# Kernel optimization log

Measured on AMD Instinct MI355X. Metric: run time of the kernel, lower is better.

Reference implementation:

```python
import jax, jax.numpy as jnp
import numpy as np

EPS = 1e-12  # layer_norm_eps

def _ln(h, g, b):
    m = jnp.mean(h, axis=-1, keepdims=True)
    v = jnp.var(h, axis=-1, keepdims=True)
    return (h - m) / jnp.sqrt(v + EPS) * g + b

def setup_inputs() -> dict:
    key = jax.random.key(0)
    B, L, C, N = 32, 512, 256, 16
    ks = jax.random.split(key, 8)
    f = jax.random.normal
    return {
        'query': f(ks[0], (B, L, C), jnp.float32),
        'x': f(ks[1], (B, L, C), jnp.float32),
        'offset': f(ks[2], (B, L, 2 * N), jnp.float32) * 0.1,
        'w1': f(ks[3], (L, L // 4), jnp.float32) * 0.02, 'b1': jnp.zeros((L // 4,), jnp.float32),
        'g1': jnp.ones((L // 4,), jnp.float32), 'bt1': jnp.zeros((L // 4,), jnp.float32),
        'w2': f(ks[4], (L // 4, L), jnp.float32) * 0.02, 'b2': jnp.zeros((L,), jnp.float32),
        'w3': f(ks[5], (C, C), jnp.float32) * 0.02, 'b3': jnp.zeros((C,), jnp.float32),
        'g3': jnp.ones((C,), jnp.float32), 'bt3': jnp.zeros((C,), jnp.float32),
        'w4': f(ks[6], (C, 2 * N), jnp.float32) * 0.02, 'b4': jnp.zeros((2 * N,), jnp.float32),
    }

def reference(query, x, offset, w1, b1, g1, bt1, w2, b2, w3, b3, g3, bt3, w4, b4):
    B, L, C = x.shape
    N = w4.shape[1] // 2
    # sample_layer: Linear over the sequence axis (query permuted to [B,C,L])
    q = jnp.swapaxes(query, 1, 2)                                        # [B,C,L]
    q = jax.nn.gelu(_ln(q @ w1 + b1, g1, bt1), approximate=False) @ w2 + b2
    q = jnp.swapaxes(q, 1, 2)                                            # [B,L,C]
    # adjust_layer over channels -> per-step 2N offsets, tanh * 0.02
    adj = jax.nn.gelu(_ln(q @ w3 + b3, g3, bt3), approximate=False) @ w4 + b4
    adj = jnp.tanh(adj) * 0.02                                           # [B,L,2N]
    local = (offset + adj).reshape(B, L, N, 2)
    # precomputed reference points (x-coord 0, y-coord depends on query step i)
    i = jnp.arange(L, dtype=x.dtype)
    n = jnp.arange(N, dtype=x.dtype) + 0.5
    ref_y = n[None, :] * 2.0 * (i[:, None] + 1e-9) / (N * L) - 1.0       # [L,N]
    ref = jnp.stack([jnp.zeros_like(ref_y), ref_y], axis=-1)             # [L,N,2]
    pos = jnp.tanh(local + ref[None])                                    # [B,L,N,2]
    # grid_sample equivalent: input [B*L, C, H=L, W=1], align_corners=True,
    # bilinear, zero padding. With W=1 the x-coordinate always maps to col 0,
    # so only pos[...,1] matters. Causal mask zeroes keys h > query step l
    # before sampling; since bilinear sampling is linear in the input, we mask
    # the two gathered taps instead of materializing the O(B*L*L*C) tensor.
    pix = (pos[..., 1] + 1.0) * 0.5 * (L - 1)                            # [B,L,N]
    i0f = jnp.floor(pix)
    frac = pix - i0f
    i0 = i0f.astype(jnp.int32)
    i1 = i0 + 1
    lpos = jnp.arange(L, dtype=jnp.int32)[None, :, None]
    v0 = (i0 >= 0) & (i0 < L) & (i0 <= lpos)
    v1 = (i1 >= 0) & (i1 < L) & (i1 <= lpos)
    c0 = jnp.clip(i0, 0, L - 1)
    c1 = jnp.clip(i1, 0, L - 1)
    bidx = jnp.arange(B)[:, None, None]
    val0 = x[bidx, c0]                                                   # [B,L,N,C]
    val1 = x[bidx, c1]                                                   # [B,L,N,C]
    w0 = jnp.where(v0, 1.0 - frac, 0.0)
    w1_ = jnp.where(v1, frac, 0.0)
    out = w0[..., None] * val0 + w1_[..., None] * val1                   # [B,L,N,C]
    return (out, offset, pos)
```

## Files before the change

### kernel.cpp

```cpp
#include <hip/hip_runtime.h>
#include <hip/hip_fp16.h>
#include <math.h>


typedef _Float16 f16;
typedef _Float16 f16x8 __attribute__((ext_vector_type(8)));
typedef float f32x4 __attribute__((ext_vector_type(4)));

#define ZERO4 f32x4{0.f, 0.f, 0.f, 0.f}

__device__ __forceinline__ float gelu_exact(float v) {
  return 0.5f * v * (1.0f + erff(v * 0.70710678118654752f));
}

__global__ __launch_bounds__(256) void k0_prep(
    const float* __restrict__ w1, const float* __restrict__ w2,
    const float* __restrict__ w3, const float* __restrict__ w4,
    f16* __restrict__ w1T, f16* __restrict__ w2T,
    f16* __restrict__ w3T, f16* __restrict__ w4T) {
  __shared__ f16 tile[64][80];
  int blk = blockIdx.x;
  const int tid = threadIdx.x;
  const float* in; f16* out; int R, Cc, tr, tc;
  if (blk < 16)      { in = w1; out = w1T; R = 512; Cc = 128; tr = blk >> 1; tc = blk & 1; }
  else if (blk < 32) { blk -= 16; in = w2; out = w2T; R = 128; Cc = 512; tr = blk >> 3; tc = blk & 7; }
  else if (blk < 48) { blk -= 32; in = w3; out = w3T; R = 256; Cc = 256; tr = blk >> 2; tc = blk & 3; }
  else               { blk -= 48; in = w4; out = w4T; R = 256; Cc = 32;  tr = blk;      tc = 0; }
  const int r0 = tr * 64, c0 = tc * 64;
  for (int id = tid; id < 4096; id += 256) {
    int rr = id >> 6, cc = id & 63;
    if (c0 + cc < Cc) tile[cc][rr] = (f16)in[(r0 + rr) * Cc + c0 + cc];
  }
  __syncthreads();
  for (int id = tid; id < 512; id += 256) {
    int cc = id >> 3, ch = id & 7;
    if (c0 + cc < Cc)
      *(f16x8*)(out + (c0 + cc) * R + r0 + ch * 8) = *(f16x8*)&tile[cc][ch * 8];
  }
}

__global__ __launch_bounds__(256) void k12_sample(
    const float* __restrict__ query, const f16* __restrict__ w1T,
    const f16* __restrict__ w2T,
    const float* __restrict__ b1, const float* __restrict__ g1,
    const float* __restrict__ bt1, const float* __restrict__ b2,
    f16* __restrict__ qout) {
  __shared__ char pool[38912];
  const int tid = threadIdx.x;
  const int b = blockIdx.x >> 4;
  const int c0 = (blockIdx.x & 15) << 4;
  const int lane = tid & 63, w = tid >> 6;
  const int mrow = lane & 15, kg = lane >> 4;
  char* At = pool;
  char* Bt = pool + 2048;
  char* t1s = pool + 32768;
  float* sb2 = (float*)(pool + 36864);

  sb2[tid] = b2[tid];
  sb2[tid + 256] = b2[tid + 256];

  const int qll = tid >> 4, qcc = tid & 15;
  const int wrj = tid >> 3, wch = tid & 7;

  float qv[4]; f16x8 wv[4];
#pragma unroll
  for (int it = 0; it < 4; ++it) {
    qv[it] = query[(((b << 9) + 0 + qll + it * 16) << 8) + c0 + qcc];
    wv[it] = *(const f16x8*)(w1T + (wrj + it * 32) * 512 + 0 + wch * 8);
  }

  f32x4 acc[2] = {ZERO4, ZERO4};
  for (int s = 0; s < 8; ++s) {
#pragma unroll
    for (int it = 0; it < 4; ++it) {
      int ll = qll + it * 16;
      *(f16*)(At + qcc * 128 + ((2 * ll) ^ ((qcc & 7) << 4))) = (f16)qv[it];
    }
#pragma unroll
    for (int it = 0; it < 4; ++it) {
      int rj = wrj + it * 32;
      *(f16x8*)(Bt + rj * 128 + ((wch * 16) ^ ((rj & 7) << 4))) = wv[it];
    }
    __syncthreads();
    if (s < 7) {
      const int k0n = (s + 1) << 6;
#pragma unroll
      for (int it = 0; it < 4; ++it) {
        qv[it] = query[(((b << 9) + k0n + qll + it * 16) << 8) + c0 + qcc];
        wv[it] = *(const f16x8*)(w1T + (wrj + it * 32) * 512 + k0n + wch * 8);
      }
    }
#pragma unroll
    for (int kk = 0; kk < 2; ++kk) {
      f16x8 a = *(const f16x8*)(At + mrow * 128 + (((kk << 6) + (kg << 4)) ^ ((mrow & 7) << 4)));
#pragma unroll
      for (int nf = 0; nf < 2; ++nf) {
        int rn = w * 32 + nf * 16 + mrow;
        f16x8 bfr = *(const f16x8*)(Bt + rn * 128 + (((kk << 6) + (kg << 4)) ^ ((rn & 7) << 4)));
        acc[nf] = __builtin_amdgcn_mfma_f32_16x16x32_f16(a, bfr, acc[nf], 0, 0, 0);
      }
    }
    __syncthreads();
  }

  f16x8 av[8];
#pragma unroll
  for (int it = 0; it < 8; ++it)
    av[it] = *(const f16x8*)(w2T + ((tid >> 4) + it * 16) * 128 + (tid & 15) * 8);

  float (*hs)[132] = (float(*)[132])pool;
#pragma unroll
  for (int nf = 0; nf < 2; ++nf)
#pragma unroll
    for (int i = 0; i < 4; ++i)
      hs[kg * 4 + i][w * 32 + nf * 16 + mrow] = acc[nf][i];
  __syncthreads();
  {
    const int r = tid >> 4, g = tid & 15;
    float s1 = 0.f, s2 = 0.f, vals[8];
#pragma unroll
    for (int jj = 0; jj < 8; ++jj) {
      int j = g * 8 + jj;
      float v = hs[r][j] + b1[j];
      vals[jj] = v; s1 += v; s2 += v * v;
    }
#pragma unroll
    for (int m = 1; m < 16; m <<= 1) { s1 += __shfl_xor(s1, m, 64); s2 += __shfl_xor(s2, m, 64); }
    const float mean = s1 * (1.f / 128.f);
    float var = fmaxf(s2 * (1.f / 128.f) - mean * mean, 0.f);
    const float rstd = rsqrtf(var + 1e-12f);
    f16 ov[8];
#pragma unroll
    for (int jj = 0; jj < 8; ++jj) {
      int j = g * 8 + jj;
      float v = (vals[jj] - mean) * rstd * g1[j] + bt1[j];
      ov[jj] = (f16)gelu_exact(v);
    }
    __syncthreads();
    *(f16x8*)(t1s + r * 256 + ((g * 16) ^ ((r & 7) << 4))) = *(f16x8*)ov;
  }
  __syncthreads();

  char* At2 = pool;
  const int ar2 = tid >> 4, ac2 = tid & 15;
  for (int lc = 0; lc < 4; ++lc) {
#pragma unroll
    for (int it = 0; it < 8; ++it) {
      int r = ar2 + it * 16;
      *(f16x8*)(At2 + r * 256 + ((ac2 * 16) ^ ((r & 7) << 4))) = av[it];
    }
    __syncthreads();
    if (lc < 3) {
#pragma unroll
      for (int it = 0; it < 8; ++it)
        av[it] = *(const f16x8*)(w2T + ((lc + 1) * 128 + ar2 + it * 16) * 128 + ac2 * 8);
    }
    f32x4 acc2[2] = {ZERO4, ZERO4};
#pragma unroll
    for (int ks = 0; ks < 4; ++ks) {
      f16x8 bfr = *(const f16x8*)(t1s + mrow * 256 + (((ks << 6) + (kg << 4)) ^ ((mrow & 7) << 4)));
#pragma unroll
      for (int mf = 0; mf < 2; ++mf) {
        int rm = w * 32 + mf * 16 + mrow;
        f16x8 a = *(const f16x8*)(At2 + rm * 256 + (((ks << 6) + (kg << 4)) ^ ((rm & 7) << 4)));
        acc2[mf] = __builtin_amdgcn_mfma_f32_16x16x32_f16(a, bfr, acc2[mf], 0, 0, 0);
      }
    }
#pragma unroll
    for (int mf = 0; mf < 2; ++mf)
#pragma unroll
      for (int i = 0; i < 4; ++i) {
        int l = lc * 128 + w * 32 + mf * 16 + kg * 4 + i;
        qout[((b << 9) + l) * 256 + c0 + mrow] = (f16)(acc2[mf][i] + sb2[l]);
      }
    __syncthreads();
  }
}

__global__ __launch_bounds__(256) void k3_adjust(
    const f16* __restrict__ qbuf, const f16* __restrict__ w3T,
    const float* __restrict__ b3, const float* __restrict__ g3,
    const float* __restrict__ bt3, const f16* __restrict__ w4T,
    const float* __restrict__ b4, const float* __restrict__ offset,
    float* __restrict__ off_out, float* __restrict__ pos_out) {
  __shared__ char pool[34816];
  __shared__ char w4t[32 * 512];
  __shared__ float sb3[256];
  const int tid = threadIdx.x;
  const int b = blockIdx.x >> 5;
  const int l0 = (blockIdx.x & 31) << 4;
  const int lane = tid & 63, w = tid >> 6;
  const int mrow = lane & 15, kg = lane >> 4;
  char* At = pool;
  char* Bt = pool + 2048;

  for (int id = tid; id < 1024; id += 256) {
    int r = id >> 5, c = id & 31;
    f16x8 v = *(const f16x8*)(w4T + r * 256 + c * 8);
    *(f16x8*)(w4t + r * 512 + ((c * 16) ^ ((r & 7) << 4))) = v;
  }
  sb3[tid] = b3[tid];

  const int sr = tid >> 3, sc = tid & 7;
  f16x8 aq; f16x8 bq[8];
  if (tid < 128) aq = *(const f16x8*)(qbuf + ((b << 9) + l0 + sr) * 256 + 0 + sc * 8);
#pragma unroll
  for (int it = 0; it < 8; ++it)
    bq[it] = *(const f16x8*)(w3T + (sr + it * 32) * 256 + 0 + sc * 8);

  f32x4 acc[4] = {ZERO4, ZERO4, ZERO4, ZERO4};
  for (int s = 0; s < 4; ++s) {
    if (tid < 128)
      *(f16x8*)(At + sr * 128 + ((sc * 16) ^ ((sr & 7) << 4))) = aq;
#pragma unroll
    for (int it = 0; it < 8; ++it) {
      int r = sr + it * 32;
      *(f16x8*)(Bt + r * 128 + ((sc * 16) ^ ((r & 7) << 4))) = bq[it];
    }
    __syncthreads();
    if (s < 3) {
      const int k0n = (s + 1) << 6;
      if (tid < 128) aq = *(const f16x8*)(qbuf + ((b << 9) + l0 + sr) * 256 + k0n + sc * 8);
#pragma unroll
      for (int it = 0; it < 8; ++it)
        bq[it] = *(const f16x8*)(w3T + (sr + it * 32) * 256 + k0n + sc * 8);
    }
#pragma unroll
    for (int kk = 0; kk < 2; ++kk) {
      f16x8 a = *(const f16x8*)(At + mrow * 128 + (((kk << 6) + (kg << 4)) ^ ((mrow & 7) << 4)));
#pragma unroll
      for (int nf = 0; nf < 4; ++nf) {
        int rn = w * 64 + nf * 16 + mrow;
        f16x8 bfr = *(const f16x8*)(Bt + rn * 128 + (((kk << 6) + (kg << 4)) ^ ((rn & 7) << 4)));
        acc[nf] = __builtin_amdgcn_mfma_f32_16x16x32_f16(a, bfr, acc[nf], 0, 0, 0);
      }
    }
    __syncthreads();
  }
  float (*hs)[264] = (float(*)[264])pool;
  char* ts = pool + 17408;
#pragma unroll
  for (int nf = 0; nf < 4; ++nf) {
    int col = w * 64 + nf * 16 + mrow;
    float bias = sb3[col];
#pragma unroll
    for (int i = 0; i < 4; ++i)
      hs[kg * 4 + i][col] = acc[nf][i] + bias;
  }
  __syncthreads();
  {
    const int r = tid >> 4, g = tid & 15;
    float s1 = 0.f, s2 = 0.f, vals[16];
#pragma unroll
    for (int jj = 0; jj < 16; ++jj) {
      float v = hs[r][g * 16 + jj];
      vals[jj] = v; s1 += v; s2 += v * v;
    }
#pragma unroll
    for (int m = 1; m < 16; m <<= 1) { s1 += __shfl_xor(s1, m, 64); s2 += __shfl_xor(s2, m, 64); }
    const float mean = s1 * (1.f / 256.f);
    float var = fmaxf(s2 * (1.f / 256.f) - mean * mean, 0.f);
    const float rstd = rsqrtf(var + 1e-12f);
    f16 ov[16];
#pragma unroll
    for (int jj = 0; jj < 16; ++jj) {
      int kch = g * 16 + jj;
      float v = (vals[jj] - mean) * rstd * g3[kch] + bt3[kch];
      ov[jj] = (f16)gelu_exact(v);
    }
    *(f16x8*)(ts + r * 512 + ((g * 32) ^ ((r & 7) << 4))) = *(f16x8*)&ov[0];
    *(f16x8*)(ts + r * 512 + ((g * 32 + 16) ^ ((r & 7) << 4))) = *(f16x8*)&ov[8];
  }
  __syncthreads();
  if (w < 2) {
    const int n4 = w;
    f32x4 a4 = ZERO4;
#pragma unroll
    for (int ks = 0; ks < 8; ++ks) {
      f16x8 a = *(const f16x8*)(ts + mrow * 512 + (((ks << 6) + (kg << 4)) ^ ((mrow & 7) << 4)));
      int br = n4 * 16 + mrow;
      f16x8 bb = *(const f16x8*)(w4t + br * 512 + (((ks << 6) + (kg << 4)) ^ ((br & 7) << 4)));
      a4 = __builtin_amdgcn_mfma_f32_16x16x32_f16(a, bb, a4, 0, 0, 0);
    }
    const int col = n4 * 16 + mrow;
#pragma unroll
    for (int i = 0; i < 4; ++i) {
      const int row = kg * 4 + i;
      const int l = l0 + row;
      float adj = tanhf(a4[i] + b4[col]) * 0.02f;
      float padj = __shfl_xor(adj, 1, 64);
      if ((lane & 1) == 0) {
        const int n = col >> 1;
        const float2 offv = *(const float2*)(offset + (((b << 9) + l) << 5) + col);
        const float pos0v = tanhf(offv.x + adj);
        const float ref_y = ((float)n + 0.5f) * ((float)l + 1e-9f) * (1.0f / 4096.0f) - 1.0f;
        const float pos1v = tanhf(offv.y + padj + ref_y);
        *(float2*)(off_out + (((b << 9) + l) << 5) + col) = offv;
        *(float2*)(pos_out + (((b << 9) + l) << 5) + col) = make_float2(pos0v, pos1v);
      }
    }
  }
}

__global__ __launch_bounds__(256) void k4_gather(
    const float* __restrict__ x, const float* __restrict__ pos,
    float* __restrict__ outbuf) {
  const unsigned tbase = blockIdx.x * 256u + threadIdx.x;
  for (unsigned u = tbase; u < 16777216u; u += 524288u) {
    const unsigned t_idx = u >> 6;
    const unsigned cj = u & 63;
    const int b = t_idx >> 13;
    const int l = (t_idx >> 4) & 511;
    const float pos1 = pos[t_idx * 2 + 1];
    const float pix = (pos1 + 1.0f) * 0.5f * 511.0f;
    const float i0f = floorf(pix);
    const int i0 = (int)i0f;
    const float frac = pix - i0f;
    const int i1 = i0 + 1;
    const bool v0 = (i0 >= 0) && (i0 < 512) && (i0 <= l);
    const bool v1 = (i1 >= 0) && (i1 < 512) && (i1 <= l);
    const int c0 = i0 < 0 ? 0 : (i0 > 511 ? 511 : i0);
    const int c1 = i1 < 0 ? 0 : (i1 > 511 ? 511 : i1);
    const float w0  = v0 ? (1.0f - frac) : 0.0f;
    const float w1v = v1 ? frac : 0.0f;
    const f32x4* x4 = (const f32x4*)x;
    const f32x4 va = x4[(unsigned)((b << 9) + c0) * 64u + cj];
    const f32x4 vb = x4[(unsigned)((b << 9) + c1) * 64u + cj];
    f32x4 o = w0 * va + w1v * vb;
    __builtin_nontemporal_store(o, (f32x4*)outbuf + u);
  }
}

extern "C" void kernel_launch(void* const* d_in, const int* in_sizes, int n_in,
                              void* d_out, int out_size, void* d_ws, size_t ws_size,
                              hipStream_t stream) {
  const float* query  = (const float*)d_in[0];
  const float* x      = (const float*)d_in[1];
  const float* offset = (const float*)d_in[2];
  const float* w1  = (const float*)d_in[3];
  const float* b1  = (const float*)d_in[4];
  const float* g1  = (const float*)d_in[5];
  const float* bt1 = (const float*)d_in[6];
  const float* w2  = (const float*)d_in[7];
  const float* b2  = (const float*)d_in[8];
  const float* w3  = (const float*)d_in[9];
  const float* b3  = (const float*)d_in[10];
  const float* g3  = (const float*)d_in[11];
  const float* bt3 = (const float*)d_in[12];
  const float* w4  = (const float*)d_in[13];
  const float* b4  = (const float*)d_in[14];

  float* out     = (float*)d_out;
  float* off_out = out + 67108864;
  float* pos_out = off_out + 524288;

  f16* w1T = (f16*)d_ws;
  f16* w2T = w1T + 65536;
  f16* w3T = w2T + 65536;
  f16* w4T = w3T + 65536;
  f16* q   = w4T + 8192;

  k0_prep<<<52, 256, 0, stream>>>(w1, w2, w3, w4, w1T, w2T, w3T, w4T);
  k12_sample<<<512, 256, 0, stream>>>(query, w1T, w2T, b1, g1, bt1, b2, q);
  k3_adjust<<<1024, 256, 0, stream>>>(q, w3T, b3, g3, bt3, w4T, b4, offset,
                                      off_out, pos_out);
  k4_gather<<<2048, 256, 0, stream>>>(x, pos_out, out);
}
```

Measured before the change: 114.4 us.

## Fuse sample, adjust and gather into persistent kernel with atomic work queue

Replaces the three separate kernels with one persistent kernel that pulls work items from a global atomic counter. Sample items publish per-batch completion counters, and adjust items spin-wait on them, so batches can move through the stages without a grid-wide barrier. The gather now runs inside the adjust item, reading the freshly computed positions from shared memory instead of reloading them from global memory. The costs are spin-wait latency, higher shared memory use that limits occupancy, and a gather handled by only 512 blocks, which may use less memory-level parallelism than the old 2048-block launch.

```diff
diff --git a/kernel.cpp b/kernel.cpp
--- a/kernel.cpp
+++ b/kernel.cpp
@@ -39,295 +39,319 @@
   }
 }
 
-__global__ __launch_bounds__(256) void k12_sample(
-    const float* __restrict__ query, const f16* __restrict__ w1T,
-    const f16* __restrict__ w2T,
+__global__ __launch_bounds__(256, 2) void k_mega(
+    const float* __restrict__ query, const float* __restrict__ x,
+    const float* __restrict__ offset,
+    const f16* __restrict__ w1T, const f16* __restrict__ w2T,
+    const f16* __restrict__ w3T, const f16* __restrict__ w4T,
     const float* __restrict__ b1, const float* __restrict__ g1,
     const float* __restrict__ bt1, const float* __restrict__ b2,
-    f16* __restrict__ qout) {
-  __shared__ char pool[38912];
+    const float* __restrict__ b3, const float* __restrict__ g3,
+    const float* __restrict__ bt3, const float* __restrict__ b4,
+    f16* __restrict__ qbuf, float* __restrict__ out,
+    float* __restrict__ off_out, float* __restrict__ pos_out,
+    unsigned* __restrict__ counters) {
+  __shared__ __align__(16) char pool[52224];
+  __shared__ unsigned sh_item;
   const int tid = threadIdx.x;
-  const int b = blockIdx.x >> 4;
-  const int c0 = (blockIdx.x & 15) << 4;
   const int lane = tid & 63, w = tid >> 6;
   const int mrow = lane & 15, kg = lane >> 4;
-  char* At = pool;
-  char* Bt = pool + 2048;
-  char* t1s = pool + 32768;
-  float* sb2 = (float*)(pool + 36864);
-
-  sb2[tid] = b2[tid];
-  sb2[tid + 256] = b2[tid + 256];
-
-  const int qll = tid >> 4, qcc = tid & 15;
-  const int wrj = tid >> 3, wch = tid & 7;
-
-  float qv[4]; f16x8 wv[4];
-#pragma unroll
-  for (int it = 0; it < 4; ++it) {
-    qv[it] = query[(((b << 9) + 0 + qll + it * 16) << 8) + c0 + qcc];
-    wv[it] = *(const f16x8*)(w1T + (wrj + it * 32) * 512 + 0 + wch * 8);
-  }
-
-  f32x4 acc[2] = {ZERO4, ZERO4};
-  for (int s = 0; s < 8; ++s) {
-#pragma unroll
-    for (int it = 0; it < 4; ++it) {
-      int ll = qll + it * 16;
-      *(f16*)(At + qcc * 128 + ((2 * ll) ^ ((qcc & 7) << 4))) = (f16)qv[it];
+
+  while (true) {
+    __syncthreads();
+    if (tid == 0) sh_item = atomicAdd(&counters[0], 1u);
+    __syncthreads();
+    const unsigned item = sh_item;
+    if (item >= 1536u) break;
+
+    if (item < 512u) {
+      const int b = (int)(item >> 4);
+      const int c0 = (int)(item & 15) << 4;
+      char* At = pool;
+      char* Bt = pool + 2048;
+      char* t1s = pool + 32768;
+      float* sb2 = (float*)(pool + 36864);
+      sb2[tid] = b2[tid];
+      sb2[tid + 256] = b2[tid + 256];
+
+      const int qll = tid >> 4, qcc = tid & 15;
+      const int wrj = tid >> 3, wch = tid & 7;
+      float qv[4]; f16x8 wv[4];
+#pragma unroll
+      for (int it = 0; it < 4; ++it) {
+        qv[it] = query[(((b << 9) + qll + it * 16) << 8) + c0 + qcc];
+        wv[it] = *(const f16x8*)(w1T + (wrj + it * 32) * 512 + wch * 8);
+      }
+
+      f32x4 acc[2] = {ZERO4, ZERO4};
+      for (int s = 0; s < 8; ++s) {
+#pragma unroll
+        for (int it = 0; it < 4; ++it) {
+          int ll = qll + it * 16;
+          *(f16*)(At + qcc * 128 + ((2 * ll) ^ ((qcc & 7) << 4))) = (f16)qv[it];
+        }
+#pragma unroll
+        for (int it = 0; it < 4; ++it) {
+          int rj = wrj + it * 32;
+          *(f16x8*)(Bt + rj * 128 + ((wch * 16) ^ ((rj & 7) << 4))) = wv[it];
+        }
+        __syncthreads();
+        if (s < 7) {
+          const int k0n = (s + 1) << 6;
+#pragma unroll
+          for (int it = 0; it < 4; ++it) {
+            qv[it] = query[(((b << 9) + k0n + qll + it * 16) << 8) + c0 + qcc];
+            wv[it] = *(const f16x8*)(w1T + (wrj + it * 32) * 512 + k0n + wch * 8);
+          }
+        }
+#pragma unroll
+        for (int kk = 0; kk < 2; ++kk) {
+          f16x8 a = *(const f16x8*)(At + mrow * 128 + (((kk << 6) + (kg << 4)) ^ ((mrow & 7) << 4)));
+#pragma unroll
+          for (int nf = 0; nf < 2; ++nf) {
+            int rn = w * 32 + nf * 16 + mrow;
+            f16x8 bfr = *(const f16x8*)(Bt + rn * 128 + (((kk << 6) + (kg << 4)) ^ ((rn & 7) << 4)));
+            acc[nf] = __builtin_amdgcn_mfma_f32_16x16x32_f16(a, bfr, acc[nf], 0, 0, 0);
+          }
+        }
+        __syncthreads();
+      }
+
+      f16x8 av[8];
+#pragma unroll
+      for (int it = 0; it < 8; ++it)
+        av[it] = *(const f16x8*)(w2T + ((tid >> 4) + it * 16) * 128 + (tid & 15) * 8);
+
+      float (*hs)[132] = (float(*)[132])pool;
+#pragma unroll
+      for (int nf = 0; nf < 2; ++nf)
+#pragma unroll
+        for (int i = 0; i < 4; ++i)
+          hs[kg * 4 + i][w * 32 + nf * 16 + mrow] = acc[nf][i];
+      __syncthreads();
+      {
+        const int r = tid >> 4, g = tid & 15;
+        float s1 = 0.f, s2 = 0.f, vals[8];
+#pragma unroll
+        for (int jj = 0; jj < 8; ++jj) {
+          int j = g * 8 + jj;
+          float v = hs[r][j] + b1[j];
+          vals[jj] = v; s1 += v; s2 += v * v;
+        }
+#pragma unroll
+        for (int m = 1; m < 16; m <<= 1) { s1 += __shfl_xor(s1, m, 64); s2 += __shfl_xor(s2, m, 64); }
+        const float mean = s1 * (1.f / 128.f);
+        float var = fmaxf(s2 * (1.f / 128.f) - mean * mean, 0.f);
+        const float rstd = rsqrtf(var + 1e-12f);
+        f16 ov[8];
+#pragma unroll
+        for (int jj = 0; jj < 8; ++jj) {
+          int j = g * 8 + jj;
+          float v = (vals[jj] - mean) * rstd * g1[j] + bt1[j];
+          ov[jj] = (f16)gelu_exact(v);
+        }
+        __syncthreads();
+        *(f16x8*)(t1s + r * 256 + ((g * 16) ^ ((r & 7) << 4))) = *(f16x8*)ov;
+      }
+      __syncthreads();
+
+      char* At2 = pool;
+      const int ar2 = tid >> 4, ac2 = tid & 15;
+      for (int lc = 0; lc < 4; ++lc) {
+#pragma unroll
+        for (int it = 0; it < 8; ++it) {
+          int r = ar2 + it * 16;
+          *(f16x8*)(At2 + r * 256 + ((ac2 * 16) ^ ((r & 7) << 4))) = av[it];
+        }
+        __syncthreads();
+        if (lc < 3) {
+#pragma unroll
+          for (int it = 0; it < 8; ++it)
+            av[it] = *(const f16x8*)(w2T + ((lc + 1) * 128 + ar2 + it * 16) * 128 + ac2 * 8);
+        }
+        f32x4 acc2[2] = {ZERO4, ZERO4};
+#pragma unroll
+        for (int ks = 0; ks < 4; ++ks) {
+          f16x8 bfr = *(const f16x8*)(t1s + mrow * 256 + (((ks << 6) + (kg << 4)) ^ ((mrow & 7) << 4)));
+#pragma unroll
+          for (int mf = 0; mf < 2; ++mf) {
+            int rm = w * 32 + mf * 16 + mrow;
+            f16x8 a = *(const f16x8*)(At2 + rm * 256 + (((ks << 6) + (kg << 4)) ^ ((rm & 7) << 4)));
+            acc2[mf] = __builtin_amdgcn_mfma_f32_16x16x32_f16(a, bfr, acc2[mf], 0, 0, 0);
+          }
+        }
+#pragma unroll
+        for (int mf = 0; mf < 2; ++mf)
+#pragma unroll
+          for (int i = 0; i < 4; ++i) {
+            int l = lc * 128 + w * 32 + mf * 16 + kg * 4 + i;
+            qbuf[((b << 9) + l) * 256 + c0 + mrow] = (f16)(acc2[mf][i] + sb2[l]);
+          }
+        __syncthreads();
+      }
+      if (tid == 0)
+        __hip_atomic_fetch_add(&counters[1 + b], 1u, __ATOMIC_RELEASE, __HIP_MEMORY_SCOPE_AGENT);
+
+    } else {
+      const unsigned it2 = item - 512u;
+      const int b = (int)(it2 >> 5);
+      const int l0 = (int)(it2 & 31) << 4;
+      char* At = pool;
+      char* Bt = pool + 2048;
+      char* ts = pool + 17408;
+      float* posbuf = (float*)(pool + 25600);
+      char* w4t = pool + 34816;
+      float* sb3 = (float*)(pool + 51200);
+
+      for (int id = tid; id < 1024; id += 256) {
+        int r = id >> 5, c = id & 31;
+        f16x8 v = *(const f16x8*)(w4T + r * 256 + c * 8);
+        *(f16x8*)(w4t + r * 512 + ((c * 16) ^ ((r & 7) << 4))) = v;
+      }
+      sb3[tid] = b3[tid];
+      const int sr = tid >> 3, sc = tid & 7;
+      f16x8 bq[8];
+#pragma unroll
+      for (int it = 0; it < 8; ++it)
+        bq[it] = *(const f16x8*)(w3T + (sr + it * 32) * 256 + sc * 8);
+
+      if (tid == 0) {
+        int spin = 0;
+        while (__hip_atomic_load(&counters[1 + b], __ATOMIC_RELAXED, __HIP_MEMORY_SCOPE_AGENT) < 16u
+               && spin < (1 << 24)) {
+          __builtin_amdgcn_s_sleep(2);
+          ++spin;
+        }
+      }
+      __syncthreads();
+      {
+        unsigned dv = __hip_atomic_load(&counters[1 + b], __ATOMIC_ACQUIRE, __HIP_MEMORY_SCOPE_AGENT);
+        asm volatile("" :: "v"(dv) : "memory");
+      }
+
+      f16x8 aq;
+      if (tid < 128) aq = *(const f16x8*)(qbuf + ((b << 9) + l0 + sr) * 256 + sc * 8);
+
+      f32x4 acc[4] = {ZERO4, ZERO4, ZERO4, ZERO4};
+      for (int s = 0; s < 4; ++s) {
+        if (tid < 128)
+          *(f16x8*)(At + sr * 128 + ((sc * 16) ^ ((sr & 7) << 4))) = aq;
+#pragma unroll
+        for (int it = 0; it < 8; ++it) {
+          int r = sr + it * 32;
+          *(f16x8*)(Bt + r * 128 + ((sc * 16) ^ ((r & 7) << 4))) = bq[it];
+        }
+        __syncthreads();
+        if (s < 3) {
+          const int k0n = (s + 1) << 6;
+          if (tid < 128) aq = *(const f16x8*)(qbuf + ((b << 9) + l0 + sr) * 256 + k0n + sc * 8);
+#pragma unroll
+          for (int it = 0; it < 8; ++it)
+            bq[it] = *(const f16x8*)(w3T + (sr + it * 32) * 256 + k0n + sc * 8);
+        }
+#pragma unroll
+        for (int kk = 0; kk < 2; ++kk) {
+          f16x8 a = *(const f16x8*)(At + mrow * 128 + (((kk << 6) + (kg << 4)) ^ ((mrow & 7) << 4)));
+#pragma unroll
+          for (int nf = 0; nf < 4; ++nf) {
+            int rn = w * 64 + nf * 16 + mrow;
+            f16x8 bfr = *(const f16x8*)(Bt + rn * 128 + (((kk << 6) + (kg << 4)) ^ ((rn & 7) << 4)));
+            acc[nf] = __builtin_amdgcn_mfma_f32_16x16x32_f16(a, bfr, acc[nf], 0, 0, 0);
+          }
+        }
+        __syncthreads();
+      }
+      float (*hs)[264] = (float(*)[264])pool;
+#pragma unroll
+      for (int nf = 0; nf < 4; ++nf) {
+        int col = w * 64 + nf * 16 + mrow;
+        float bias = sb3[col];
+#pragma unroll
+        for (int i = 0; i < 4; ++i)
+          hs[kg * 4 + i][col] = acc[nf][i] + bias;
+      }
+      __syncthreads();
+      {
+        const int r = tid >> 4, g = tid & 15;
+        float s1 = 0.f, s2 = 0.f, vals[16];
+#pragma unroll
+        for (int jj = 0; jj < 16; ++jj) {
+          float v = hs[r][g * 16 + jj];
+          vals[jj] = v; s1 += v; s2 += v * v;
+        }
+#pragma unroll
+        for (int m = 1; m < 16; m <<= 1) { s1 += __shfl_xor(s1, m, 64); s2 += __shfl_xor(s2, m, 64); }
+        const float mean = s1 * (1.f / 256.f);
+        float var = fmaxf(s2 * (1.f / 256.f) - mean * mean, 0.f);
+        const float rstd = rsqrtf(var + 1e-12f);
+        f16 ov[16];
+#pragma unroll
+        for (int jj = 0; jj < 16; ++jj) {
+          int kch = g * 16 + jj;
+          float v = (vals[jj] - mean) * rstd * g3[kch] + bt3[kch];
+          ov[jj] = (f16)gelu_exact(v);
+        }
+        *(f16x8*)(ts + r * 512 + ((g * 32) ^ ((r & 7) << 4))) = *(f16x8*)&ov[0];
+        *(f16x8*)(ts + r * 512 + ((g * 32 + 16) ^ ((r & 7) << 4))) = *(f16x8*)&ov[8];
+      }
+      __syncthreads();
+      if (w < 2) {
+        const int n4 = w;
+        f32x4 a4 = ZERO4;
+#pragma unroll
+        for (int ks = 0; ks < 8; ++ks) {
+          f16x8 a = *(const f16x8*)(ts + mrow * 512 + (((ks << 6) + (kg << 4)) ^ ((mrow & 7) << 4)));
+          int br = n4 * 16 + mrow;
+          f16x8 bb = *(const f16x8*)(w4t + br * 512 + (((ks << 6) + (kg << 4)) ^ ((br & 7) << 4)));
+          a4 = __builtin_amdgcn_mfma_f32_16x16x32_f16(a, bb, a4, 0, 0, 0);
+        }
+        const int col = n4 * 16 + mrow;
+#pragma unroll
+        for (int i = 0; i < 4; ++i) {
+          const int row = kg * 4 + i;
+          const int l = l0 + row;
+          float adj = tanhf(a4[i] + b4[col]) * 0.02f;
+          float padj = __shfl_xor(adj, 1, 64);
+          if ((lane & 1) == 0) {
+            const int n = col >> 1;
+            const float2 offv = *(const float2*)(offset + (((b << 9) + l) << 5) + col);
+            const float pos0v = tanhf(offv.x + adj);
+            const float ref_y = ((float)n + 0.5f) * ((float)l + 1e-9f) * (1.0f / 4096.0f) - 1.0f;
+            const float pos1v = tanhf(offv.y + padj + ref_y);
+            *(float2*)(off_out + (((b << 9) + l) << 5) + col) = offv;
+            *(float2*)(pos_out + (((b << 9) + l) << 5) + col) = make_float2(pos0v, pos1v);
+            posbuf[row * 16 + n] = pos1v;
+          }
+        }
+      }
+      __syncthreads();
+      {
+        const f32x4* x4 = (const f32x4*)x;
+        f32x4* out4 = (f32x4*)out;
+#pragma unroll 2
+        for (int it = 0; it < 64; ++it) {
+          const int idx = w * 64 + it;
+          const int lloc = idx >> 4, n = idx & 15;
+          const float pos1 = posbuf[lloc * 16 + n];
+          const int l = l0 + lloc;
+          const float pix = (pos1 + 1.0f) * 0.5f * 511.0f;
+          const float i0f = floorf(pix);
+          const int i0 = (int)i0f;
+          const float frac = pix - i0f;
+          const int i1 = i0 + 1;
+          const bool v0 = (i0 >= 0) && (i0 < 512) && (i0 <= l);
+          const bool v1 = (i1 >= 0) && (i1 < 512) && (i1 <= l);
+          const int cc0 = i0 < 0 ? 0 : (i0 > 511 ? 511 : i0);
+          const int cc1 = i1 < 0 ? 0 : (i1 > 511 ? 511 : i1);
+          const float w0  = v0 ? (1.0f - frac) : 0.0f;
+          const float w1v = v1 ? frac : 0.0f;
+          const f32x4 va = x4[(unsigned)((b << 9) + cc0) * 64u + lane];
+          const f32x4 vb = x4[(unsigned)((b << 9) + cc1) * 64u + lane];
+          f32x4 o = w0 * va + w1v * vb;
+          __builtin_nontemporal_store(o, out4 + ((unsigned)(((b << 9) + l) * 16 + n) * 64u + lane));
+        }
+      }
     }
-#pragma unroll
-    for (int it = 0; it < 4; ++it) {
-      int rj = wrj + it * 32;
-      *(f16x8*)(Bt + rj * 128 + ((wch * 16) ^ ((rj & 7) << 4))) = wv[it];
-    }
-    __syncthreads();
-    if (s < 7) {
-      const int k0n = (s + 1) << 6;
-#pragma unroll
-      for (int it = 0; it < 4; ++it) {
-        qv[it] = query[(((b << 9) + k0n + qll + it * 16) << 8) + c0 + qcc];
-        wv[it] = *(const f16x8*)(w1T + (wrj + it * 32) * 512 + k0n + wch * 8);
-      }
-    }
-#pragma unroll
-    for (int kk = 0; kk < 2; ++kk) {
-      f16x8 a = *(const f16x8*)(At + mrow * 128 + (((kk << 6) + (kg << 4)) ^ ((mrow & 7) << 4)));
-#pragma unroll
-      for (int nf = 0; nf < 2; ++nf) {
-        int rn = w * 32 + nf * 16 + mrow;
-        f16x8 bfr = *(const f16x8*)(Bt + rn * 128 + (((kk << 6) + (kg << 4)) ^ ((rn & 7) << 4)));
-        acc[nf] = __builtin_amdgcn_mfma_f32_16x16x32_f16(a, bfr, acc[nf], 0, 0, 0);
-      }
-    }
-    __syncthreads();
-  }
-
-  f16x8 av[8];
-#pragma unroll
-  for (int it = 0; it < 8; ++it)
-    av[it] = *(const f16x8*)(w2T + ((tid >> 4) + it * 16) * 128 + (tid & 15) * 8);
-
-  float (*hs)[132] = (float(*)[132])pool;
-#pragma unroll
-  for (int nf = 0; nf < 2; ++nf)
-#pragma unroll
-    for (int i = 0; i < 4; ++i)
-      hs[kg * 4 + i][w * 32 + nf * 16 + mrow] = acc[nf][i];
-  __syncthreads();
-  {
-    const int r = tid >> 4, g = tid & 15;
-    float s1 = 0.f, s2 = 0.f, vals[8];
-#pragma unroll
-    for (int jj = 0; jj < 8; ++jj) {
-      int j = g * 8 + jj;
-      float v = hs[r][j] + b1[j];
-      vals[jj] = v; s1 += v; s2 += v * v;
-    }
-#pragma unroll
-    for (int m = 1; m < 16; m <<= 1) { s1 += __shfl_xor(s1, m, 64); s2 += __shfl_xor(s2, m, 64); }
-    const float mean = s1 * (1.f / 128.f);
-    float var = fmaxf(s2 * (1.f / 128.f) - mean * mean, 0.f);
-    const float rstd = rsqrtf(var + 1e-12f);
-    f16 ov[8];
-#pragma unroll
-    for (int jj = 0; jj < 8; ++jj) {
-      int j = g * 8 + jj;
-      float v = (vals[jj] - mean) * rstd * g1[j] + bt1[j];
-      ov[jj] = (f16)gelu_exact(v);
-    }
-    __syncthreads();
-    *(f16x8*)(t1s + r * 256 + ((g * 16) ^ ((r & 7) << 4))) = *(f16x8*)ov;
-  }
-  __syncthreads();
-
-  char* At2 = pool;
-  const int ar2 = tid >> 4, ac2 = tid & 15;
-  for (int lc = 0; lc < 4; ++lc) {
-#pragma unroll
-    for (int it = 0; it < 8; ++it) {
-      int r = ar2 + it * 16;
-      *(f16x8*)(At2 + r * 256 + ((ac2 * 16) ^ ((r & 7) << 4))) = av[it];
-    }
-    __syncthreads();
-    if (lc < 3) {
-#pragma unroll
-      for (int it = 0; it < 8; ++it)
-        av[it] = *(const f16x8*)(w2T + ((lc + 1) * 128 + ar2 + it * 16) * 128 + ac2 * 8);
-    }
-    f32x4 acc2[2] = {ZERO4, ZERO4};
-#pragma unroll
-    for (int ks = 0; ks < 4; ++ks) {
-      f16x8 bfr = *(const f16x8*)(t1s + mrow * 256 + (((ks << 6) + (kg << 4)) ^ ((mrow & 7) << 4)));
-#pragma unroll
-      for (int mf = 0; mf < 2; ++mf) {
-        int rm = w * 32 + mf * 16 + mrow;
-        f16x8 a = *(const f16x8*)(At2 + rm * 256 + (((ks << 6) + (kg << 4)) ^ ((rm & 7) << 4)));
-        acc2[mf] = __builtin_amdgcn_mfma_f32_16x16x32_f16(a, bfr, acc2[mf], 0, 0, 0);
-      }
-    }
-#pragma unroll
-    for (int mf = 0; mf < 2; ++mf)
-#pragma unroll
-      for (int i = 0; i < 4; ++i) {
-        int l = lc * 128 + w * 32 + mf * 16 + kg * 4 + i;
-        qout[((b << 9) + l) * 256 + c0 + mrow] = (f16)(acc2[mf][i] + sb2[l]);
-      }
-    __syncthreads();
-  }
-}
-
-__global__ __launch_bounds__(256) void k3_adjust(
-    const f16* __restrict__ qbuf, const f16* __restrict__ w3T,
-    const float* __restrict__ b3, const float* __restrict__ g3,
-    const float* __restrict__ bt3, const f16* __restrict__ w4T,
-    const float* __restrict__ b4, const float* __restrict__ offset,
-    float* __restrict__ off_out, float* __restrict__ pos_out) {
-  __shared__ char pool[34816];
-  __shared__ char w4t[32 * 512];
-  __shared__ float sb3[256];
-  const int tid = threadIdx.x;
-  const int b = blockIdx.x >> 5;
-  const int l0 = (blockIdx.x & 31) << 4;
-  const int lane = tid & 63, w = tid >> 6;
-  const int mrow = lane & 15, kg = lane >> 4;
-  char* At = pool;
-  char* Bt = pool + 2048;
-
-  for (int id = tid; id < 1024; id += 256) {
-    int r = id >> 5, c = id & 31;
-    f16x8 v = *(const f16x8*)(w4T + r * 256 + c * 8);
-    *(f16x8*)(w4t + r * 512 + ((c * 16) ^ ((r & 7) << 4))) = v;
-  }
-  sb3[tid] = b3[tid];
-
-  const int sr = tid >> 3, sc = tid & 7;
-  f16x8 aq; f16x8 bq[8];
-  if (tid < 128) aq = *(const f16x8*)(qbuf + ((b << 9) + l0 + sr) * 256 + 0 + sc * 8);
-#pragma unroll
-  for (int it = 0; it < 8; ++it)
-    bq[it] = *(const f16x8*)(w3T + (sr + it * 32) * 256 + 0 + sc * 8);
-
-  f32x4 acc[4] = {ZERO4, ZERO4, ZERO4, ZERO4};
-  for (int s = 0; s < 4; ++s) {
-    if (tid < 128)
-      *(f16x8*)(At + sr * 128 + ((sc * 16) ^ ((sr & 7) << 4))) = aq;
-#pragma unroll
-    for (int it = 0; it < 8; ++it) {
-      int r = sr + it * 32;
-      *(f16x8*)(Bt + r * 128 + ((sc * 16) ^ ((r & 7) << 4))) = bq[it];
-    }
-    __syncthreads();
-    if (s < 3) {
-      const int k0n = (s + 1) << 6;
-      if (tid < 128) aq = *(const f16x8*)(qbuf + ((b << 9) + l0 + sr) * 256 + k0n + sc * 8);
-#pragma unroll
-      for (int it = 0; it < 8; ++it)
-        bq[it] = *(const f16x8*)(w3T + (sr + it * 32) * 256 + k0n + sc * 8);
-    }
-#pragma unroll
-    for (int kk = 0; kk < 2; ++kk) {
-      f16x8 a = *(const f16x8*)(At + mrow * 128 + (((kk << 6) + (kg << 4)) ^ ((mrow & 7) << 4)));
-#pragma unroll
-      for (int nf = 0; nf < 4; ++nf) {
-        int rn = w * 64 + nf * 16 + mrow;
-        f16x8 bfr = *(const f16x8*)(Bt + rn * 128 + (((kk << 6) + (kg << 4)) ^ ((rn & 7) << 4)));
-        acc[nf] = __builtin_amdgcn_mfma_f32_16x16x32_f16(a, bfr, acc[nf], 0, 0, 0);
-      }
-    }
-    __syncthreads();
-  }
-  float (*hs)[264] = (float(*)[264])pool;
-  char* ts = pool + 17408;
-#pragma unroll
-  for (int nf = 0; nf < 4; ++nf) {
-    int col = w * 64 + nf * 16 + mrow;
-    float bias = sb3[col];
-#pragma unroll
-    for (int i = 0; i < 4; ++i)
-      hs[kg * 4 + i][col] = acc[nf][i] + bias;
-  }
-  __syncthreads();
-  {
-    const int r = tid >> 4, g = tid & 15;
-    float s1 = 0.f, s2 = 0.f, vals[16];
-#pragma unroll
-    for (int jj = 0; jj < 16; ++jj) {
-      float v = hs[r][g * 16 + jj];
-      vals[jj] = v; s1 += v; s2 += v * v;
-    }
-#pragma unroll
-    for (int m = 1; m < 16; m <<= 1) { s1 += __shfl_xor(s1, m, 64); s2 += __shfl_xor(s2, m, 64); }
-    const float mean = s1 * (1.f / 256.f);
-    float var = fmaxf(s2 * (1.f / 256.f) - mean * mean, 0.f);
-    const float rstd = rsqrtf(var + 1e-12f);
-    f16 ov[16];
-#pragma unroll
-    for (int jj = 0; jj < 16; ++jj) {
-      int kch = g * 16 + jj;
-      float v = (vals[jj] - mean) * rstd * g3[kch] + bt3[kch];
-      ov[jj] = (f16)gelu_exact(v);
-    }
-    *(f16x8*)(ts + r * 512 + ((g * 32) ^ ((r & 7) << 4))) = *(f16x8*)&ov[0];
-    *(f16x8*)(ts + r * 512 + ((g * 32 + 16) ^ ((r & 7) << 4))) = *(f16x8*)&ov[8];
-  }
-  __syncthreads();
-  if (w < 2) {
-    const int n4 = w;
-    f32x4 a4 = ZERO4;
-#pragma unroll
-    for (int ks = 0; ks < 8; ++ks) {
-      f16x8 a = *(const f16x8*)(ts + mrow * 512 + (((ks << 6) + (kg << 4)) ^ ((mrow & 7) << 4)));
-      int br = n4 * 16 + mrow;
-      f16x8 bb = *(const f16x8*)(w4t + br * 512 + (((ks << 6) + (kg << 4)) ^ ((br & 7) << 4)));
-      a4 = __builtin_amdgcn_mfma_f32_16x16x32_f16(a, bb, a4, 0, 0, 0);
-    }
-    const int col = n4 * 16 + mrow;
-#pragma unroll
-    for (int i = 0; i < 4; ++i) {
-      const int row = kg * 4 + i;
-      const int l = l0 + row;
-      float adj = tanhf(a4[i] + b4[col]) * 0.02f;
-      float padj = __shfl_xor(adj, 1, 64);
-      if ((lane & 1) == 0) {
-        const int n = col >> 1;
-        const float2 offv = *(const float2*)(offset + (((b << 9) + l) << 5) + col);
-        const float pos0v = tanhf(offv.x + adj);
-        const float ref_y = ((float)n + 0.5f) * ((float)l + 1e-9f) * (1.0f / 4096.0f) - 1.0f;
-        const float pos1v = tanhf(offv.y + padj + ref_y);
-        *(float2*)(off_out + (((b << 9) + l) << 5) + col) = offv;
-        *(float2*)(pos_out + (((b << 9) + l) << 5) + col) = make_float2(pos0v, pos1v);
-      }
-    }
-  }
-}
-
-__global__ __launch_bounds__(256) void k4_gather(
-    const float* __restrict__ x, const float* __restrict__ pos,
-    float* __restrict__ outbuf) {
-  const unsigned tbase = blockIdx.x * 256u + threadIdx.x;
-  for (unsigned u = tbase; u < 16777216u; u += 524288u) {
-    const unsigned t_idx = u >> 6;
-    const unsigned cj = u & 63;
-    const int b = t_idx >> 13;
-    const int l = (t_idx >> 4) & 511;
-    const float pos1 = pos[t_idx * 2 + 1];
-    const float pix = (pos1 + 1.0f) * 0.5f * 511.0f;
-    const float i0f = floorf(pix);
-    const int i0 = (int)i0f;
-    const float frac = pix - i0f;
-    const int i1 = i0 + 1;
-    const bool v0 = (i0 >= 0) && (i0 < 512) && (i0 <= l);
-    const bool v1 = (i1 >= 0) && (i1 < 512) && (i1 <= l);
-    const int c0 = i0 < 0 ? 0 : (i0 > 511 ? 511 : i0);
-    const int c1 = i1 < 0 ? 0 : (i1 > 511 ? 511 : i1);
-    const float w0  = v0 ? (1.0f - frac) : 0.0f;
-    const float w1v = v1 ? frac : 0.0f;
-    const f32x4* x4 = (const f32x4*)x;
-    const f32x4 va = x4[(unsigned)((b << 9) + c0) * 64u + cj];
-    const f32x4 vb = x4[(unsigned)((b << 9) + c1) * 64u + cj];
-    f32x4 o = w0 * va + w1v * vb;
-    __builtin_nontemporal_store(o, (f32x4*)outbuf + u);
   }
 }
 
@@ -354,15 +378,16 @@
   float* off_out = out + 67108864;
   float* pos_out = off_out + 524288;
 
-  f16* w1T = (f16*)d_ws;
+  unsigned* counters = (unsigned*)d_ws;
+  f16* w1T = (f16*)((char*)d_ws + 256);
   f16* w2T = w1T + 65536;
   f16* w3T = w2T + 65536;
   f16* w4T = w3T + 65536;
   f16* q   = w4T + 8192;
 
+  hipMemsetAsync(counters, 0, 256, stream);
   k0_prep<<<52, 256, 0, stream>>>(w1, w2, w3, w4, w1T, w2T, w3T, w4T);
-  k12_sample<<<512, 256, 0, stream>>>(query, w1T, w2T, b1, g1, bt1, b2, q);
-  k3_adjust<<<1024, 256, 0, stream>>>(q, w3T, b3, g3, bt3, w4T, b4, offset,
-                                      off_out, pos_out);
-  k4_gather<<<2048, 256, 0, stream>>>(x, pos_out, out);
+  k_mega<<<512, 256, 0, stream>>>(query, x, offset, w1T, w2T, w3T, w4T,
+                                  b1, g1, bt1, b2, b3, g3, bt3, b4,
+                                  q, out, off_out, pos_out, counters);
 }
```

Measured after the change: 215.2 us. 88.1% more time.

## Fuse adjust MLP and bilinear gather into one kernel, drop LDS staging

Applied to the files above, without the earlier changes.

Merges the adjust-layer kernel and the gather kernel so each block computes pos for its 16 rows, keeps pos1 in shared memory, and then directly gathers and writes the corresponding output rows. This removes one launch and the global round trip of pos for the gather. The w3/w4 GEMM operands are now read straight from global memory into MFMA fragments instead of being staged through swizzled LDS. A launch-bounds occupancy hint is also added. The trade-off is that the bandwidth-heavy 256MB output store now runs with only 1024 blocks, each doing GEMM work first, which may hurt how well memory traffic overlaps.

```diff
diff --git a/kernel.cpp b/kernel.cpp
--- a/kernel.cpp
+++ b/kernel.cpp
@@ -61,12 +61,11 @@
 
   const int qll = tid >> 4, qcc = tid & 15;
   const int wrj = tid >> 3, wch = tid & 7;
-
   float qv[4]; f16x8 wv[4];
 #pragma unroll
   for (int it = 0; it < 4; ++it) {
-    qv[it] = query[(((b << 9) + 0 + qll + it * 16) << 8) + c0 + qcc];
-    wv[it] = *(const f16x8*)(w1T + (wrj + it * 32) * 512 + 0 + wch * 8);
+    qv[it] = query[(((b << 9) + qll + it * 16) << 8) + c0 + qcc];
+    wv[it] = *(const f16x8*)(w1T + (wrj + it * 32) * 512 + wch * 8);
   }
 
   f32x4 acc[2] = {ZERO4, ZERO4};
@@ -177,68 +176,39 @@
   }
 }
 
-__global__ __launch_bounds__(256) void k3_adjust(
+__global__ __launch_bounds__(256, 4) void k3_fused(
     const f16* __restrict__ qbuf, const f16* __restrict__ w3T,
     const float* __restrict__ b3, const float* __restrict__ g3,
     const float* __restrict__ bt3, const f16* __restrict__ w4T,
     const float* __restrict__ b4, const float* __restrict__ offset,
+    const float* __restrict__ x, float* __restrict__ out,
     float* __restrict__ off_out, float* __restrict__ pos_out) {
-  __shared__ char pool[34816];
-  __shared__ char w4t[32 * 512];
-  __shared__ float sb3[256];
+  __shared__ __align__(16) char pool[27648];
   const int tid = threadIdx.x;
   const int b = blockIdx.x >> 5;
   const int l0 = (blockIdx.x & 31) << 4;
   const int lane = tid & 63, w = tid >> 6;
   const int mrow = lane & 15, kg = lane >> 4;
-  char* At = pool;
-  char* Bt = pool + 2048;
-
-  for (int id = tid; id < 1024; id += 256) {
-    int r = id >> 5, c = id & 31;
-    f16x8 v = *(const f16x8*)(w4T + r * 256 + c * 8);
-    *(f16x8*)(w4t + r * 512 + ((c * 16) ^ ((r & 7) << 4))) = v;
-  }
-  sb3[tid] = b3[tid];
-
-  const int sr = tid >> 3, sc = tid & 7;
-  f16x8 aq; f16x8 bq[8];
-  if (tid < 128) aq = *(const f16x8*)(qbuf + ((b << 9) + l0 + sr) * 256 + 0 + sc * 8);
-#pragma unroll
-  for (int it = 0; it < 8; ++it)
-    bq[it] = *(const f16x8*)(w3T + (sr + it * 32) * 256 + 0 + sc * 8);
-
-  f32x4 acc[4] = {ZERO4, ZERO4, ZERO4, ZERO4};
-  for (int s = 0; s < 4; ++s) {
-    if (tid < 128)
-      *(f16x8*)(At + sr * 128 + ((sc * 16) ^ ((sr & 7) << 4))) = aq;
-#pragma unroll
-    for (int it = 0; it < 8; ++it) {
-      int r = sr + it * 32;
-      *(f16x8*)(Bt + r * 128 + ((sc * 16) ^ ((r & 7) << 4))) = bq[it];
-    }
-    __syncthreads();
-    if (s < 3) {
-      const int k0n = (s + 1) << 6;
-      if (tid < 128) aq = *(const f16x8*)(qbuf + ((b << 9) + l0 + sr) * 256 + k0n + sc * 8);
-#pragma unroll
-      for (int it = 0; it < 8; ++it)
-        bq[it] = *(const f16x8*)(w3T + (sr + it * 32) * 256 + k0n + sc * 8);
-    }
-#pragma unroll
-    for (int kk = 0; kk < 2; ++kk) {
-      f16x8 a = *(const f16x8*)(At + mrow * 128 + (((kk << 6) + (kg << 4)) ^ ((mrow & 7) << 4)));
-#pragma unroll
-      for (int nf = 0; nf < 4; ++nf) {
-        int rn = w * 64 + nf * 16 + mrow;
-        f16x8 bfr = *(const f16x8*)(Bt + rn * 128 + (((kk << 6) + (kg << 4)) ^ ((rn & 7) << 4)));
-        acc[nf] = __builtin_amdgcn_mfma_f32_16x16x32_f16(a, bfr, acc[nf], 0, 0, 0);
-      }
-    }
-    __syncthreads();
-  }
   float (*hs)[264] = (float(*)[264])pool;
   char* ts = pool + 17408;
+  float* posbuf = (float*)(pool + 25600);
+  float* sb3 = (float*)(pool + 26624);
+
+  sb3[tid] = b3[tid];
+
+  f32x4 acc[4] = {ZERO4, ZERO4, ZERO4, ZERO4};
+  const f16* arow = qbuf + ((b << 9) + l0 + mrow) * 256 + kg * 8;
+#pragma unroll
+  for (int kf = 0; kf < 8; ++kf) {
+    f16x8 a = *(const f16x8*)(arow + kf * 32);
+#pragma unroll
+    for (int nf = 0; nf < 4; ++nf) {
+      int rn = w * 64 + nf * 16 + mrow;
+      f16x8 bb = *(const f16x8*)(w3T + rn * 256 + kf * 32 + kg * 8);
+      acc[nf] = __builtin_amdgcn_mfma_f32_16x16x32_f16(a, bb, acc[nf], 0, 0, 0);
+    }
+  }
+  __syncthreads();
 #pragma unroll
   for (int nf = 0; nf < 4; ++nf) {
     int col = w * 64 + nf * 16 + mrow;
@@ -279,7 +249,7 @@
     for (int ks = 0; ks < 8; ++ks) {
       f16x8 a = *(const f16x8*)(ts + mrow * 512 + (((ks << 6) + (kg << 4)) ^ ((mrow & 7) << 4)));
       int br = n4 * 16 + mrow;
-      f16x8 bb = *(const f16x8*)(w4t + br * 512 + (((ks << 6) + (kg << 4)) ^ ((br & 7) << 4)));
+      f16x8 bb = *(const f16x8*)(w4T + br * 256 + ks * 32 + kg * 8);
       a4 = __builtin_amdgcn_mfma_f32_16x16x32_f16(a, bb, a4, 0, 0, 0);
     }
     const int col = n4 * 16 + mrow;
@@ -297,37 +267,36 @@
         const float pos1v = tanhf(offv.y + padj + ref_y);
         *(float2*)(off_out + (((b << 9) + l) << 5) + col) = offv;
         *(float2*)(pos_out + (((b << 9) + l) << 5) + col) = make_float2(pos0v, pos1v);
-      }
-    }
-  }
-}
-
-__global__ __launch_bounds__(256) void k4_gather(
-    const float* __restrict__ x, const float* __restrict__ pos,
-    float* __restrict__ outbuf) {
-  const unsigned tbase = blockIdx.x * 256u + threadIdx.x;
-  for (unsigned u = tbase; u < 16777216u; u += 524288u) {
-    const unsigned t_idx = u >> 6;
-    const unsigned cj = u & 63;
-    const int b = t_idx >> 13;
-    const int l = (t_idx >> 4) & 511;
-    const float pos1 = pos[t_idx * 2 + 1];
-    const float pix = (pos1 + 1.0f) * 0.5f * 511.0f;
-    const float i0f = floorf(pix);
-    const int i0 = (int)i0f;
-    const float frac = pix - i0f;
-    const int i1 = i0 + 1;
-    const bool v0 = (i0 >= 0) && (i0 < 512) && (i0 <= l);
-    const bool v1 = (i1 >= 0) && (i1 < 512) && (i1 <= l);
-    const int c0 = i0 < 0 ? 0 : (i0 > 511 ? 511 : i0);
-    const int c1 = i1 < 0 ? 0 : (i1 > 511 ? 511 : i1);
-    const float w0  = v0 ? (1.0f - frac) : 0.0f;
-    const float w1v = v1 ? frac : 0.0f;
+        posbuf[row * 16 + n] = pos1v;
+      }
+    }
+  }
+  __syncthreads();
+  {
     const f32x4* x4 = (const f32x4*)x;
-    const f32x4 va = x4[(unsigned)((b << 9) + c0) * 64u + cj];
-    const f32x4 vb = x4[(unsigned)((b << 9) + c1) * 64u + cj];
-    f32x4 o = w0 * va + w1v * vb;
-    __builtin_nontemporal_store(o, (f32x4*)outbuf + u);
+    f32x4* out4 = (f32x4*)out;
+#pragma unroll 8
+    for (int it = 0; it < 64; ++it) {
+      const int idx = w * 64 + it;
+      const int lloc = idx >> 4, n = idx & 15;
+      const float pos1 = posbuf[lloc * 16 + n];
+      const int l = l0 + lloc;
+      const float pix = (pos1 + 1.0f) * 0.5f * 511.0f;
+      const float i0f = floorf(pix);
+      const int i0 = (int)i0f;
+      const float frac = pix - i0f;
+      const int i1 = i0 + 1;
+      const bool v0 = (i0 >= 0) && (i0 < 512) && (i0 <= l);
+      const bool v1 = (i1 >= 0) && (i1 < 512) && (i1 <= l);
+      const int cc0 = i0 < 0 ? 0 : (i0 > 511 ? 511 : i0);
+      const int cc1 = i1 < 0 ? 0 : (i1 > 511 ? 511 : i1);
+      const float w0  = v0 ? (1.0f - frac) : 0.0f;
+      const float w1v = v1 ? frac : 0.0f;
+      const f32x4 va = x4[(unsigned)((b << 9) + cc0) * 64u + lane];
+      const f32x4 vb = x4[(unsigned)((b << 9) + cc1) * 64u + lane];
+      f32x4 o = w0 * va + w1v * vb;
+      __builtin_nontemporal_store(o, out4 + ((unsigned)(((b << 9) + l) * 16 + n) * 64u + lane));
+    }
   }
 }
 
@@ -362,7 +331,6 @@
 
   k0_prep<<<52, 256, 0, stream>>>(w1, w2, w3, w4, w1T, w2T, w3T, w4T);
   k12_sample<<<512, 256, 0, stream>>>(query, w1T, w2T, b1, g1, bt1, b2, q);
-  k3_adjust<<<1024, 256, 0, stream>>>(q, w3T, b3, g3, bt3, w4T, b4, offset,
-                                      off_out, pos_out);
-  k4_gather<<<2048, 256, 0, stream>>>(x, pos_out, out);
-}
+  k3_fused<<<1024, 256, 0, stream>>>(q, w3T, b3, g3, bt3, w4T, b4, offset,
+                                     x, out, off_out, pos_out);
+}
```

New measurement: 122.1 us. 6.7% more time.
